# Kernel optimization log

Measured on AMD Instinct MI355X. Metric: run time of the kernel, lower is better.

Reference implementation:

```python
import jax, jax.numpy as jnp
import numpy as np

ATTWSIZE = 64  # sliding window length (matches init_kwargs attwsize)


def setup_inputs() -> dict:
    key = jax.random.key(0)
    k1, k2, k3 = jax.random.split(key, 3)
    B, T, D, A = 32, 4096, 256, 128
    x = jax.random.normal(k1, (B, T, D), dtype=jnp.float32)
    Wp = jax.random.normal(k2, (A, D), dtype=jnp.float32) / np.sqrt(D).astype(np.float32)
    bp = jnp.zeros((A,), dtype=jnp.float32)
    Wg = jax.random.normal(k3, (1, A), dtype=jnp.float32) / np.sqrt(A).astype(np.float32)
    return {"x": x, "Wp": Wp, "bp": bp, "Wg": Wg}


def _windowed_sum(v, w):
    # causal sliding-window sum over axis=1: sum(v[:, max(t-w+1,0):t+1, :])
    # single-pass cumsum formulation: cs[t] - cs[t-w]
    cs = jnp.cumsum(v, axis=1)
    T = v.shape[1]
    shifted = jnp.pad(cs, ((0, 0), (w, 0), (0, 0)))[:, :T, :]
    return cs - shifted


def reference(x, Wp, bp, Wg):
    # proj = tanh(Linear(dimio->dimatt)(x))
    proj = jnp.tanh(jnp.einsum('btd,ad->bta', x, Wp) + bp)
    # gvec = sigmoid(Linear(dimatt->1, no bias)(proj))  -> [B, T, 1]
    g = jax.nn.sigmoid(jnp.einsum('bta,oa->bto', proj, Wg))
    wx = g * x  # gated input [B, T, D]
    num = _windowed_sum(wx, ATTWSIZE)         # [B, T, D]
    den = _windowed_sum(g, ATTWSIZE)          # [B, T, 1] broadcasts over D
    return num / den
```

## Files before the change

kernel.cpp:

```cpp
#include <hip/hip_runtime.h>

#define TT 4096
#define DD 256
#define AA 128
#define WIN 64

typedef short bf16x8 __attribute__((ext_vector_type(8)));
typedef float f32x4 __attribute__((ext_vector_type(4)));
typedef unsigned int u32x4 __attribute__((ext_vector_type(4)));

__device__ __forceinline__ unsigned short f2bf(float f) {
    unsigned int u = __builtin_bit_cast(unsigned int, f);
    u += 0x7FFFu + ((u >> 16) & 1u);
    return (unsigned short)(u >> 16);
}

__device__ __forceinline__ unsigned int cvt_pk_bf16(float lo, float hi) {
    unsigned int r;
    asm("v_cvt_pk_bf16_f32 %0, %1, %2" : "=v"(r) : "v"(lo), "v"(hi));
    return r;
}

__global__ __launch_bounds__(256) void prep_wp(const float* __restrict__ Wp,
                                               unsigned short* __restrict__ wpb) {
    int i = blockIdx.x * 256 + threadIdx.x;
    wpb[i] = f2bf(Wp[i]);
}

#define RTILE 128
#define SROWS 32
#define NSUB  (RTILE / SROWS)

__global__ __launch_bounds__(256, 2) void gate_kernel(
        const float* __restrict__ x, const unsigned short* __restrict__ wpb,
        const float* __restrict__ bp, const float* __restrict__ Wg,
        float* __restrict__ g) {
    __shared__ __align__(16) float xs[2][SROWS * DD];
    __shared__ float psum[4][SROWS];
    const int tid  = threadIdx.x;
    const int lane = tid & 63;
    const int wave = tid >> 6;
    const int quad = lane >> 4;
    const int nrow = lane & 15;
    const int sw   = nrow & 7;
    const long row0 = (long)blockIdx.x * RTILE;
    const float* xbase = x + row0 * DD;

    bf16x8 bfrag[2][8];
    float bpv[2], wgv[2];
#pragma unroll
    for (int nt = 0; nt < 2; ++nt) {
        int n = wave * 32 + nt * 16 + nrow;
        bpv[nt] = bp[n];
        wgv[nt] = Wg[n];
#pragma unroll
        for (int k0 = 0; k0 < 8; ++k0)
            bfrag[nt][k0] = *reinterpret_cast<const bf16x8*>(
                wpb + n * DD + k0 * 32 + quad * 8);
    }

    auto stage = [&](int nb, int s) {
        const float* src = xbase + (long)s * SROWS * DD;
#pragma unroll
        for (int j = 0; j < 8; ++j) {
            int r = wave * 8 + j;
            const float* gp = src + r * DD + ((lane ^ (r & 7)) << 2);
            __builtin_amdgcn_global_load_lds(
                (const __attribute__((address_space(1))) void*)gp,
                (__attribute__((address_space(3))) void*)&xs[nb][r * DD],
                16, 0, 0);
        }
    };

    stage(0, 0);
    __syncthreads();

    for (int s = 0; s < NSUB; ++s) {
        if (s + 1 < NSUB) stage((s + 1) & 1, s + 1);
        const int cur = s & 1;

        f32x4 acc[2][2];
#pragma unroll
        for (int mt = 0; mt < 2; ++mt)
#pragma unroll
            for (int nt = 0; nt < 2; ++nt)
                acc[mt][nt] = (f32x4){0.f, 0.f, 0.f, 0.f};

#pragma unroll
        for (int k0 = 0; k0 < 8; ++k0) {
#pragma unroll
            for (int mt = 0; mt < 2; ++mt) {
                const float* rowp = &xs[cur][(mt * 16 + nrow) * DD];
                const int gidx = quad * 2 + k0 * 8;
                float4 f0 = *reinterpret_cast<const float4*>(rowp + (((gidx)     ^ sw) << 2));
                float4 f1 = *reinterpret_cast<const float4*>(rowp + (((gidx + 1) ^ sw) << 2));
                u32x4 w;
                w.x = cvt_pk_bf16(f0.x, f0.y);
                w.y = cvt_pk_bf16(f0.z, f0.w);
                w.z = cvt_pk_bf16(f1.x, f1.y);
                w.w = cvt_pk_bf16(f1.z, f1.w);
                bf16x8 af = __builtin_bit_cast(bf16x8, w);
                acc[mt][0] = __builtin_amdgcn_mfma_f32_16x16x32_bf16(af, bfrag[0][k0], acc[mt][0], 0, 0, 0);
                acc[mt][1] = __builtin_amdgcn_mfma_f32_16x16x32_bf16(af, bfrag[1][k0], acc[mt][1], 0, 0, 0);
            }
        }

        float p[2][4];
#pragma unroll
        for (int mt = 0; mt < 2; ++mt)
#pragma unroll
            for (int r = 0; r < 4; ++r) p[mt][r] = 0.f;
#pragma unroll
        for (int nt = 0; nt < 2; ++nt) {
#pragma unroll
            for (int mt = 0; mt < 2; ++mt) {
#pragma unroll
                for (int r = 0; r < 4; ++r) {
                    float pre = acc[mt][nt][r] + bpv[nt];
                    float e  = __expf(2.0f * pre);
                    float th = 1.0f - 2.0f * __builtin_amdgcn_rcpf(e + 1.0f);
                    p[mt][r] += th * wgv[nt];
                }
            }
        }
#pragma unroll
        for (int off = 1; off <= 8; off <<= 1)
#pragma unroll
            for (int mt = 0; mt < 2; ++mt)
#pragma unroll
                for (int r = 0; r < 4; ++r)
                    p[mt][r] += __shfl_xor(p[mt][r], off, 64);
        if (nrow == 0) {
#pragma unroll
            for (int mt = 0; mt < 2; ++mt)
#pragma unroll
                for (int r = 0; r < 4; ++r)
                    psum[wave][mt * 16 + quad * 4 + r] = p[mt][r];
        }
        __syncthreads();
        if (tid < SROWS) {
            float ssum = psum[0][tid] + psum[1][tid] + psum[2][tid] + psum[3][tid];
            g[row0 + s * SROWS + tid] = __builtin_amdgcn_rcpf(1.0f + __expf(-ssum));
        }
        __syncthreads();
    }
}

#define TC 128
#define NCHUNK (TT / TC)

__global__ __launch_bounds__(256) void stream_kernel(
        const float* __restrict__ x, const float* __restrict__ g,
        float* __restrict__ out) {
    __shared__ float gbuf[2][TC + WIN];
    const int grp  = threadIdx.x >> 7;
    const int d2   = threadIdx.x & 127;
    const int pair = blockIdx.x * 2 + grp;
    const int b     = pair >> 5;
    const int chunk = pair & (NCHUNK - 1);
    const int t0    = chunk * TC;
    const float2* xb2 = reinterpret_cast<const float2*>(x + (size_t)b * TT * DD);
    const float*  gb  = g + (size_t)b * TT;
    float2* ob2 = reinterpret_cast<float2*>(out + (size_t)b * TT * DD);

    for (int i = d2; i < TC + WIN; i += 128) {
        int s = t0 - WIN + i;
        gbuf[grp][i] = (s >= 0) ? gb[s] : 0.f;
    }
    __syncthreads();

    float2 S = {0.f, 0.f};
    float Sg = 0.f;
#pragma unroll 16
    for (int i = 0; i < WIN; ++i) {
        int s  = t0 - WIN + i;
        int sc = s < 0 ? 0 : s;
        float gv = gbuf[grp][i];
        float2 xv = xb2[(size_t)sc * (DD / 2) + d2];
        S.x += gv * xv.x;
        S.y += gv * xv.y;
        Sg  += gv;
    }

#pragma unroll 8
    for (int tt = 0; tt < TC; ++tt) {
        int t   = t0 + tt;
        int ts  = t - WIN;
        int tsc = ts < 0 ? 0 : ts;
        float gnew = gbuf[grp][WIN + tt];
        float gold = gbuf[grp][tt];
        float2 xn = xb2[(size_t)t   * (DD / 2) + d2];
        float2 xo = xb2[(size_t)tsc * (DD / 2) + d2];
        S.x += gnew * xn.x - gold * xo.x;
        S.y += gnew * xn.y - gold * xo.y;
        Sg  += gnew - gold;
        float r = __builtin_amdgcn_rcpf(Sg);
        float2 o; o.x = S.x * r; o.y = S.y * r;
        ob2[(size_t)t * (DD / 2) + d2] = o;
    }
}

extern "C" void kernel_launch(void* const* d_in, const int* in_sizes, int n_in,
                              void* d_out, int out_size, void* d_ws, size_t ws_size,
                              hipStream_t stream) {
    const float* x  = (const float*)d_in[0];
    const float* Wp = (const float*)d_in[1];
    const float* bp = (const float*)d_in[2];
    const float* Wg = (const float*)d_in[3];
    float* out = (float*)d_out;

    unsigned short* wpb = (unsigned short*)d_ws;
    float* g = (float*)((char*)d_ws + 65536);

    prep_wp<<<AA * DD / 256, 256, 0, stream>>>(Wp, wpb);
    gate_kernel<<<32 * TT / RTILE, 256, 0, stream>>>(x, wpb, bp, Wg, g);
    stream_kernel<<<32 * NCHUNK / 2, 256, 0, stream>>>(x, g, out);
}
```

Measured before the change: 299.5 us.

## Triple-buffer gate kernel x staging with vmcnt waits and larger row blocks

The gate kernel now processes 512 rows per block instead of 128 and uses a three-deep LDS ring buffer. Explicit vmcnt waits let two async global-to-LDS loads stay in flight while the current tile is computed. Per-subtile gate reductions are deferred into a larger psum array and finalized once at the end, which removes the two __syncthreads per subtile. In exchange it cuts the grid to 256 blocks at one block per CU and uses more LDS, so occupancy falls and the vmcnt counts are tied to the exact number of loads per stage.

```diff
diff --git a/kernel.cpp b/kernel.cpp
--- a/kernel.cpp
+++ b/kernel.cpp
@@ -21,29 +21,36 @@
     return r;
 }
 
+template <int W> __device__ __forceinline__ void waitcnt_vm() {
+    if constexpr (W == 16)      asm volatile("s_waitcnt vmcnt(16)" ::: "memory");
+    else if constexpr (W == 8)  asm volatile("s_waitcnt vmcnt(8)"  ::: "memory");
+    else                        asm volatile("s_waitcnt vmcnt(0)"  ::: "memory");
+    __builtin_amdgcn_sched_barrier(0);
+}
+
 __global__ __launch_bounds__(256) void prep_wp(const float* __restrict__ Wp,
                                                unsigned short* __restrict__ wpb) {
     int i = blockIdx.x * 256 + threadIdx.x;
     wpb[i] = f2bf(Wp[i]);
 }
 
-#define RTILE 128
 #define SROWS 32
-#define NSUB  (RTILE / SROWS)
-
-__global__ __launch_bounds__(256, 2) void gate_kernel(
+#define BROWS 512
+#define NSUB  (BROWS / SROWS)
+
+__global__ __launch_bounds__(256, 1) void gate_kernel(
         const float* __restrict__ x, const unsigned short* __restrict__ wpb,
         const float* __restrict__ bp, const float* __restrict__ Wg,
         float* __restrict__ g) {
-    __shared__ __align__(16) float xs[2][SROWS * DD];
-    __shared__ float psum[4][SROWS];
+    __shared__ __align__(16) float xs[3][SROWS * DD];
+    __shared__ float psum[4][BROWS];
     const int tid  = threadIdx.x;
     const int lane = tid & 63;
     const int wave = tid >> 6;
     const int quad = lane >> 4;
     const int nrow = lane & 15;
     const int sw   = nrow & 7;
-    const long row0 = (long)blockIdx.x * RTILE;
+    const long row0 = (long)blockIdx.x * BROWS;
     const float* xbase = x + row0 * DD;
 
     bf16x8 bfrag[2][8];
@@ -72,13 +79,7 @@
         }
     };
 
-    stage(0, 0);
-    __syncthreads();
-
-    for (int s = 0; s < NSUB; ++s) {
-        if (s + 1 < NSUB) stage((s + 1) & 1, s + 1);
-        const int cur = s & 1;
-
+    auto compute = [&](const float* buf, int s) {
         f32x4 acc[2][2];
 #pragma unroll
         for (int mt = 0; mt < 2; ++mt)
@@ -90,7 +91,7 @@
         for (int k0 = 0; k0 < 8; ++k0) {
 #pragma unroll
             for (int mt = 0; mt < 2; ++mt) {
-                const float* rowp = &xs[cur][(mt * 16 + nrow) * DD];
+                const float* rowp = buf + (mt * 16 + nrow) * DD;
                 const int gidx = quad * 2 + k0 * 8;
                 float4 f0 = *reinterpret_cast<const float4*>(rowp + (((gidx)     ^ sw) << 2));
                 float4 f1 = *reinterpret_cast<const float4*>(rowp + (((gidx + 1) ^ sw) << 2));
@@ -135,14 +136,37 @@
             for (int mt = 0; mt < 2; ++mt)
 #pragma unroll
                 for (int r = 0; r < 4; ++r)
-                    psum[wave][mt * 16 + quad * 4 + r] = p[mt][r];
-        }
-        __syncthreads();
-        if (tid < SROWS) {
-            float ssum = psum[0][tid] + psum[1][tid] + psum[2][tid] + psum[3][tid];
-            g[row0 + s * SROWS + tid] = __builtin_amdgcn_rcpf(1.0f + __expf(-ssum));
-        }
-        __syncthreads();
+                    psum[wave][s * 32 + mt * 16 + quad * 4 + r] = p[mt][r];
+        }
+    };
+
+    stage(0, 0);
+    stage(1, 1);
+    stage(2, 2);
+
+    int bi = 0;
+    for (int s = 0; s < NSUB; ++s) {
+        if (s < NSUB - 2)       waitcnt_vm<16>();
+        else if (s == NSUB - 2) waitcnt_vm<8>();
+        else                    waitcnt_vm<0>();
+        __builtin_amdgcn_s_barrier();
+        __builtin_amdgcn_sched_barrier(0);
+
+        compute(xs[bi], s);
+
+        __builtin_amdgcn_sched_barrier(0);
+        asm volatile("s_waitcnt lgkmcnt(0)" ::: "memory");
+        __builtin_amdgcn_sched_barrier(0);
+        __builtin_amdgcn_s_barrier();
+        __builtin_amdgcn_sched_barrier(0);
+
+        if (s < NSUB - 3) stage(bi, s + 3);
+        bi = (bi == 2) ? 0 : bi + 1;
+    }
+
+    for (int i = tid; i < BROWS; i += 256) {
+        float ssum = psum[0][i] + psum[1][i] + psum[2][i] + psum[3][i];
+        g[row0 + i] = __builtin_amdgcn_rcpf(1.0f + __expf(-ssum));
     }
 }
 
@@ -213,6 +237,6 @@
     float* g = (float*)((char*)d_ws + 65536);
 
     prep_wp<<<AA * DD / 256, 256, 0, stream>>>(Wp, wpb);
-    gate_kernel<<<32 * TT / RTILE, 256, 0, stream>>>(x, wpb, bp, Wg, g);
+    gate_kernel<<<32 * TT / BROWS, 256, 0, stream>>>(x, wpb, bp, Wg, g);
     stream_kernel<<<32 * NCHUNK / 2, 256, 0, stream>>>(x, g, out);
 }
```

Result: no change. 303.9 us (+1.5%).

## Fuse gate computation and sliding-window stream into one kernel

Applied to the files above, without the earlier changes.

Merges the gate GEMM kernel and the windowed-sum kernel into a single kernel. Each block owns a 512-row chunk of one batch plus a 64-row halo, staged through a 4-deep LDS ring. Gates are computed per 32-row tile, and the running window sum is updated directly from the staged LDS tiles. This removes the second global read of x and the global round trip for g. In exchange it runs only 256 blocks at one block per CU, recomputes the halo gates, and serialises each block through many barriers, which can limit latency hiding.

```diff
diff --git a/kernel.cpp b/kernel.cpp
--- a/kernel.cpp
+++ b/kernel.cpp
@@ -27,15 +27,17 @@
     wpb[i] = f2bf(Wp[i]);
 }
 
-#define RTILE 128
 #define SROWS 32
-#define NSUB  (RTILE / SROWS)
-
-__global__ __launch_bounds__(256, 2) void gate_kernel(
+#define TC    512
+#define NU    ((TC + WIN) / SROWS)
+#define NCHK  (TT / TC)
+
+__global__ __launch_bounds__(256, 1) void fused_kernel(
         const float* __restrict__ x, const unsigned short* __restrict__ wpb,
         const float* __restrict__ bp, const float* __restrict__ Wg,
-        float* __restrict__ g) {
-    __shared__ __align__(16) float xs[2][SROWS * DD];
+        float* __restrict__ out) {
+    __shared__ __align__(16) float xs[4][SROWS * DD];
+    __shared__ float gbuf[4][SROWS];
     __shared__ float psum[4][SROWS];
     const int tid  = threadIdx.x;
     const int lane = tid & 63;
@@ -43,8 +45,11 @@
     const int quad = lane >> 4;
     const int nrow = lane & 15;
     const int sw   = nrow & 7;
-    const long row0 = (long)blockIdx.x * RTILE;
-    const float* xbase = x + row0 * DD;
+    const int b     = blockIdx.x >> 3;
+    const int chunk = blockIdx.x & (NCHK - 1);
+    const long t0   = (long)chunk * TC;
+    const float* xb = x   + (size_t)b * TT * DD;
+    float*       ob = out + (size_t)b * TT * DD;
 
     bf16x8 bfrag[2][8];
     float bpv[2], wgv[2];
@@ -59,12 +64,15 @@
                 wpb + n * DD + k0 * 32 + quad * 8);
     }
 
-    auto stage = [&](int nb, int s) {
-        const float* src = xbase + (long)s * SROWS * DD;
+    auto stage = [&](int u) {
+        const int nb = u & 3;
+        const long r0 = t0 - WIN + (long)u * SROWS;
 #pragma unroll
         for (int j = 0; j < 8; ++j) {
             int r = wave * 8 + j;
-            const float* gp = src + r * DD + ((lane ^ (r & 7)) << 2);
+            long row = r0 + r;
+            row = row < 0 ? 0 : row;
+            const float* gp = xb + row * DD + ((lane ^ (r & 7)) << 2);
             __builtin_amdgcn_global_load_lds(
                 (const __attribute__((address_space(1))) void*)gp,
                 (__attribute__((address_space(3))) void*)&xs[nb][r * DD],
@@ -72,25 +80,29 @@
         }
     };
 
-    stage(0, 0);
-    __syncthreads();
-
-    for (int s = 0; s < NSUB; ++s) {
-        if (s + 1 < NSUB) stage((s + 1) & 1, s + 1);
-        const int cur = s & 1;
-
+    float S = 0.f, Sg = 0.f;
+
+    stage(0);
+    asm volatile("s_waitcnt vmcnt(0)" ::: "memory");
+    __builtin_amdgcn_sched_barrier(0);
+    __builtin_amdgcn_s_barrier();
+    __builtin_amdgcn_sched_barrier(0);
+
+    for (int u = 0; u < NU; ++u) {
+        if (u + 1 < NU) stage(u + 1);
+
+        const float* buf = xs[u & 3];
         f32x4 acc[2][2];
 #pragma unroll
         for (int mt = 0; mt < 2; ++mt)
 #pragma unroll
             for (int nt = 0; nt < 2; ++nt)
                 acc[mt][nt] = (f32x4){0.f, 0.f, 0.f, 0.f};
-
 #pragma unroll
         for (int k0 = 0; k0 < 8; ++k0) {
 #pragma unroll
             for (int mt = 0; mt < 2; ++mt) {
-                const float* rowp = &xs[cur][(mt * 16 + nrow) * DD];
+                const float* rowp = buf + (mt * 16 + nrow) * DD;
                 const int gidx = quad * 2 + k0 * 8;
                 float4 f0 = *reinterpret_cast<const float4*>(rowp + (((gidx)     ^ sw) << 2));
                 float4 f1 = *reinterpret_cast<const float4*>(rowp + (((gidx + 1) ^ sw) << 2));
@@ -104,7 +116,6 @@
                 acc[mt][1] = __builtin_amdgcn_mfma_f32_16x16x32_bf16(af, bfrag[1][k0], acc[mt][1], 0, 0, 0);
             }
         }
-
         float p[2][4];
 #pragma unroll
         for (int mt = 0; mt < 2; ++mt)
@@ -137,66 +148,54 @@
                 for (int r = 0; r < 4; ++r)
                     psum[wave][mt * 16 + quad * 4 + r] = p[mt][r];
         }
-        __syncthreads();
+
+        asm volatile("s_waitcnt lgkmcnt(0)" ::: "memory");
+        __builtin_amdgcn_sched_barrier(0);
+        __builtin_amdgcn_s_barrier();
+        __builtin_amdgcn_sched_barrier(0);
+
         if (tid < SROWS) {
             float ssum = psum[0][tid] + psum[1][tid] + psum[2][tid] + psum[3][tid];
-            g[row0 + s * SROWS + tid] = __builtin_amdgcn_rcpf(1.0f + __expf(-ssum));
-        }
-        __syncthreads();
-    }
-}
-
-#define TC 128
-#define NCHUNK (TT / TC)
-
-__global__ __launch_bounds__(256) void stream_kernel(
-        const float* __restrict__ x, const float* __restrict__ g,
-        float* __restrict__ out) {
-    __shared__ float gbuf[2][TC + WIN];
-    const int grp  = threadIdx.x >> 7;
-    const int d2   = threadIdx.x & 127;
-    const int pair = blockIdx.x * 2 + grp;
-    const int b     = pair >> 5;
-    const int chunk = pair & (NCHUNK - 1);
-    const int t0    = chunk * TC;
-    const float2* xb2 = reinterpret_cast<const float2*>(x + (size_t)b * TT * DD);
-    const float*  gb  = g + (size_t)b * TT;
-    float2* ob2 = reinterpret_cast<float2*>(out + (size_t)b * TT * DD);
-
-    for (int i = d2; i < TC + WIN; i += 128) {
-        int s = t0 - WIN + i;
-        gbuf[grp][i] = (s >= 0) ? gb[s] : 0.f;
-    }
-    __syncthreads();
-
-    float2 S = {0.f, 0.f};
-    float Sg = 0.f;
-#pragma unroll 16
-    for (int i = 0; i < WIN; ++i) {
-        int s  = t0 - WIN + i;
-        int sc = s < 0 ? 0 : s;
-        float gv = gbuf[grp][i];
-        float2 xv = xb2[(size_t)sc * (DD / 2) + d2];
-        S.x += gv * xv.x;
-        S.y += gv * xv.y;
-        Sg  += gv;
-    }
-
+            float gg = __builtin_amdgcn_rcpf(1.0f + __expf(-ssum));
+            long row = t0 - WIN + (long)u * SROWS + tid;
+            gbuf[u & 3][tid] = (row < 0) ? 0.f : gg;
+        }
+        asm volatile("s_waitcnt lgkmcnt(0)" ::: "memory");
+        __builtin_amdgcn_sched_barrier(0);
+        __builtin_amdgcn_s_barrier();
+        __builtin_amdgcn_sched_barrier(0);
+
+        if (u >= 2) {
+            const int v  = u - 2;
+            const int bn = u & 3, bo = v & 3;
+            const float* fn = xs[bn];
+            const float* fo = xs[bo];
+            const long tbase = t0 + (long)v * SROWS;
 #pragma unroll 8
-    for (int tt = 0; tt < TC; ++tt) {
-        int t   = t0 + tt;
-        int ts  = t - WIN;
-        int tsc = ts < 0 ? 0 : ts;
-        float gnew = gbuf[grp][WIN + tt];
-        float gold = gbuf[grp][tt];
-        float2 xn = xb2[(size_t)t   * (DD / 2) + d2];
-        float2 xo = xb2[(size_t)tsc * (DD / 2) + d2];
-        S.x += gnew * xn.x - gold * xo.x;
-        S.y += gnew * xn.y - gold * xo.y;
-        Sg  += gnew - gold;
-        float r = __builtin_amdgcn_rcpf(Sg);
-        float2 o; o.x = S.x * r; o.y = S.y * r;
-        ob2[(size_t)t * (DD / 2) + d2] = o;
+            for (int tt = 0; tt < SROWS; ++tt) {
+                int off = tt * DD + ((((tid >> 2) ^ (tt & 7)) << 2) | (tid & 3));
+                float gnew = gbuf[bn][tt];
+                float gold = gbuf[bo][tt];
+                S  += gnew * fn[off] - gold * fo[off];
+                Sg += gnew - gold;
+                ob[(tbase + tt) * DD + tid] = S * __builtin_amdgcn_rcpf(Sg);
+            }
+        } else {
+            const int bn = u & 3;
+            const float* fn = xs[bn];
+#pragma unroll 8
+            for (int tt = 0; tt < SROWS; ++tt) {
+                int off = tt * DD + ((((tid >> 2) ^ (tt & 7)) << 2) | (tid & 3));
+                float gnew = gbuf[bn][tt];
+                S  += gnew * fn[off];
+                Sg += gnew;
+            }
+        }
+
+        asm volatile("s_waitcnt vmcnt(0)" ::: "memory");
+        __builtin_amdgcn_sched_barrier(0);
+        __builtin_amdgcn_s_barrier();
+        __builtin_amdgcn_sched_barrier(0);
     }
 }
 
@@ -210,9 +209,7 @@
     float* out = (float*)d_out;
 
     unsigned short* wpb = (unsigned short*)d_ws;
-    float* g = (float*)((char*)d_ws + 65536);
 
     prep_wp<<<AA * DD / 256, 256, 0, stream>>>(Wp, wpb);
-    gate_kernel<<<32 * TT / RTILE, 256, 0, stream>>>(x, wpb, bp, Wg, g);
-    stream_kernel<<<32 * NCHUNK / 2, 256, 0, stream>>>(x, g, out);
-}
+    fused_kernel<<<32 * NCHK, 256, 0, stream>>>(x, wpb, bp, Wg, out);
+}
```

Result: faster. 266.3 us (-11.1%).
